# Kernel optimization log

Hardware: AMD Instinct MI355X
Metric: run time of the kernel (lower is better)

The kernel has to match this reference:

```python
import jax, jax.numpy as jnp
import numpy as np

M = 12          # persons per frame
K = 2           # partition channels from conv1da (1024 = 2*512)
D = 512         # GCN channel dim / LSTM hidden
C_IN = 4096     # backbone feature dim
NUM_CLASSES = 8


def setup_inputs() -> dict:
    key = jax.random.key(0)
    ks = jax.random.split(key, 8)
    N, T = 16, 32
    NT = N * T
    base_out = jax.random.normal(ks[0], (NT, M, C_IN), dtype=jnp.float32)
    dist = jax.random.uniform(ks[1], (N, T, 3, K, M, M), dtype=jnp.float32)
    # conv1da: Conv1d(4096 -> 1024, k=1, bias=False) == matmul with [1024, 4096]
    w_a = jax.random.normal(ks[2], (K * D, C_IN), dtype=jnp.float32) * 0.02
    # LSTM(512, 512, 1): torch gate order i, f, g, o
    s = 1.0 / np.sqrt(D)
    w_ih = jax.random.uniform(ks[3], (4 * D, D), minval=-s, maxval=s, dtype=jnp.float32)
    w_hh = jax.random.uniform(ks[4], (4 * D, D), minval=-s, maxval=s, dtype=jnp.float32)
    b_ih = jax.random.uniform(ks[5], (4 * D,), minval=-s, maxval=s, dtype=jnp.float32)
    b_hh = jax.random.uniform(ks[6], (4 * D,), minval=-s, maxval=s, dtype=jnp.float32)
    # gclassifier: Linear(512 -> num_classes)
    w_cls = jax.random.normal(ks[7], (NUM_CLASSES, D), dtype=jnp.float32) * 0.01
    b_cls = jnp.zeros((NUM_CLASSES,), dtype=jnp.float32)
    return {"base_out": base_out, "dist": dist, "w_a": w_a,
            "w_ih": w_ih, "w_hh": w_hh, "b_ih": b_ih, "b_hh": b_hh,
            "w_cls": w_cls, "b_cls": b_cls, "n_videos": N}


def reference(base_out, dist, w_a, w_ih, w_hh, b_ih, b_hh, w_cls, b_cls, n_videos):
    NT = base_out.shape[0]
    N = n_videos
    T = NT // N
    # conv1da (1x1 conv, no bias): [NT, M, 4096] -> [NT, K*D, M] -> [NT, K, D, M]
    node1 = jnp.einsum('nmc,oc->nom', base_out, w_a).reshape(NT, K, D, M)
    # fused three-way adjacency aggregation: node1a + node1b + node1c
    A = (dist[:, :, 2] + dist[:, :, 1] + dist[:, :, 0]).reshape(NT, K, M, M)
    node = jnp.einsum('nkcv,nkvw->ncw', node1, A)  # [NT, D, M]
    node = jax.nn.relu(node)
    # AdaptiveAvgPool1d(1) over the M persons
    pooled = node.mean(axis=2)                      # [NT, D]
    seq = pooled.reshape(N, T, D)
    # torch nn.LSTM default batch_first=False: iterates over axis 0 (N), batch=T
    def step(carry, x_t):
        h, c = carry
        g = x_t @ w_ih.T + b_ih + h @ w_hh.T + b_hh  # [T, 4D]
        i, f, gg, o = jnp.split(g, 4, axis=-1)
        c = jax.nn.sigmoid(f) * c + jax.nn.sigmoid(i) * jnp.tanh(gg)
        h = jax.nn.sigmoid(o) * jnp.tanh(c)
        return (h, c), h
    h0 = jnp.zeros((T, D), dtype=seq.dtype)
    c0 = jnp.zeros((T, D), dtype=seq.dtype)
    _, hs = jax.lax.scan(step, (h0, c0), seq)       # [N, T, D]
    last = hs[:, -1, :]                              # video_feat[:, -1, :]
    return last @ w_cls.T + b_cls                    # [N, num_classes]
```

## Files before the change

### kernel.cpp

```cpp
#include <hip/hip_runtime.h>
#include <math.h>

#define MM 12
#define KK 2
#define DD 512
#define CIN 4096
#define NCLS 8
#define NV 16
#define TT 32

typedef unsigned long long u64;
typedef __attribute__((ext_vector_type(8))) __bf16 bf16x8;
typedef __attribute__((ext_vector_type(4))) float f32x4;

#define PART_F   0
#define POOLED_F 786432
#define TAGA_F   794624
#define TAGD_F   798720
#define HGLOB_F  799232
#define PART_KS_STRIDE (192 * 1024)

#define MFMA_BF16(A, B, C) __builtin_amdgcn_mfma_f32_16x16x32_bf16((A), (B), (C), 0, 0, 0)
#define LOADR(p)      __hip_atomic_load((p), __ATOMIC_RELAXED, __HIP_MEMORY_SCOPE_AGENT)
#define LOADACQ(p)    __hip_atomic_load((p), __ATOMIC_ACQUIRE, __HIP_MEMORY_SCOPE_AGENT)
#define STORER(p, v)  __hip_atomic_store((p), (v), __ATOMIC_RELAXED, __HIP_MEMORY_SCOPE_AGENT)
#define STOREREL(p, v) __hip_atomic_store((p), (v), __ATOMIC_RELEASE, __HIP_MEMORY_SCOPE_AGENT)

__global__ __launch_bounds__(256, 1) void k_gemm_pool(
    const float* __restrict__ base_out, const float* __restrict__ dist,
    const float* __restrict__ w_a,
    float* __restrict__ part, float* __restrict__ pooled,
    unsigned* __restrict__ tagA)
{
  const int wg = blockIdx.x;
  const int tid = threadIdx.x;

  __shared__ __align__(16) unsigned short Ah[16 * 40], Al[16 * 40];
  __shared__ __align__(16) unsigned short Bh[192 * 40], Bl[192 * 40];
  __shared__ float Asum_s[KK * MM * MM];

  {
    const int ks = wg >> 6, ot = wg & 63;
    const int cc0 = ks * 1024;
    const int wave = tid >> 6, lane = tid & 63;
    const int jf0 = wave * 3;

    const int sq = tid & 7;
    const int sr = tid >> 3;
    unsigned boff[6];
#pragma unroll
    for (int rep = 0; rep < 6; ++rep) {
      const int j = sr + 32 * rep;
      const int n = j / 12, m = j - n * 12;
      boff[rep] = (unsigned)(((n * TT + 31) * MM + m) * CIN + cc0 + sq * 4);
    }
    const bool aact = tid < 128;
    unsigned aoff = aact ? (unsigned)((ot * 16 + (tid >> 3)) * CIN + cc0 + sq * 4) : 0u;

    f32x4 acc0 = {0.f, 0.f, 0.f, 0.f}, acc1 = acc0, acc2 = acc0;

    float4 pa, pb[6];
    if (aact) pa = *(const float4*)&w_a[aoff];
#pragma unroll
    for (int rep = 0; rep < 6; ++rep) pb[rep] = *(const float4*)&base_out[boff[rep]];

    for (int st = 0; st < 32; ++st) {
      __syncthreads();
      if (aact) {
        const int idx = (tid >> 3) * 40 + sq * 4;
        unsigned ux = __float_as_uint(pa.x), uy = __float_as_uint(pa.y);
        unsigned uz = __float_as_uint(pa.z), uw = __float_as_uint(pa.w);
        *(uint2*)&Ah[idx] = make_uint2((ux >> 16) | (uy & 0xFFFF0000u),
                                       (uz >> 16) | (uw & 0xFFFF0000u));
        unsigned lx = __float_as_uint(pa.x - __uint_as_float(ux & 0xFFFF0000u));
        unsigned ly = __float_as_uint(pa.y - __uint_as_float(uy & 0xFFFF0000u));
        unsigned lz = __float_as_uint(pa.z - __uint_as_float(uz & 0xFFFF0000u));
        unsigned lw = __float_as_uint(pa.w - __uint_as_float(uw & 0xFFFF0000u));
        *(uint2*)&Al[idx] = make_uint2((lx >> 16) | (ly & 0xFFFF0000u),
                                       (lz >> 16) | (lw & 0xFFFF0000u));
      }
#pragma unroll
      for (int rep = 0; rep < 6; ++rep) {
        const int idx = (sr + 32 * rep) * 40 + sq * 4;
        unsigned ux = __float_as_uint(pb[rep].x), uy = __float_as_uint(pb[rep].y);
        unsigned uz = __float_as_uint(pb[rep].z), uw = __float_as_uint(pb[rep].w);
        *(uint2*)&Bh[idx] = make_uint2((ux >> 16) | (uy & 0xFFFF0000u),
                                       (uz >> 16) | (uw & 0xFFFF0000u));
        unsigned lx = __float_as_uint(pb[rep].x - __uint_as_float(ux & 0xFFFF0000u));
        unsigned ly = __float_as_uint(pb[rep].y - __uint_as_float(uy & 0xFFFF0000u));
        unsigned lz = __float_as_uint(pb[rep].z - __uint_as_float(uz & 0xFFFF0000u));
        unsigned lw = __float_as_uint(pb[rep].w - __uint_as_float(uw & 0xFFFF0000u));
        *(uint2*)&Bl[idx] = make_uint2((lx >> 16) | (ly & 0xFFFF0000u),
                                       (lz >> 16) | (lw & 0xFFFF0000u));
      }
      __syncthreads();
      if (st < 31) {
        aoff += 32;
        if (aact) pa = *(const float4*)&w_a[aoff];
#pragma unroll
        for (int rep = 0; rep < 6; ++rep) {
          boff[rep] += 32;
          pb[rep] = *(const float4*)&base_out[boff[rep]];
        }
      }
      const int koff = (lane >> 4) * 8;
      const int fra = (lane & 15) * 40 + koff;
      bf16x8 oh = *(const bf16x8*)&Ah[fra];
      bf16x8 ol = *(const bf16x8*)&Al[fra];
      {
        const int r0 = ((jf0 + 0) * 16 + (lane & 15)) * 40 + koff;
        bf16x8 jh = *(const bf16x8*)&Bh[r0], jl = *(const bf16x8*)&Bl[r0];
        acc0 = MFMA_BF16(jh, oh, acc0);
        acc0 = MFMA_BF16(jh, ol, acc0);
        acc0 = MFMA_BF16(jl, oh, acc0);
      }
      {
        const int r1 = ((jf0 + 1) * 16 + (lane & 15)) * 40 + koff;
        bf16x8 jh = *(const bf16x8*)&Bh[r1], jl = *(const bf16x8*)&Bl[r1];
        acc1 = MFMA_BF16(jh, oh, acc1);
        acc1 = MFMA_BF16(jh, ol, acc1);
        acc1 = MFMA_BF16(jl, oh, acc1);
      }
      {
        const int r2 = ((jf0 + 2) * 16 + (lane & 15)) * 40 + koff;
        bf16x8 jh = *(const bf16x8*)&Bh[r2], jl = *(const bf16x8*)&Bl[r2];
        acc2 = MFMA_BF16(jh, oh, acc2);
        acc2 = MFMA_BF16(jh, ol, acc2);
        acc2 = MFMA_BF16(jl, oh, acc2);
      }
    }
    const int o = ot * 16 + (lane & 15);
    const int jr = (lane >> 4) * 4;
#pragma unroll
    for (int r = 0; r < 4; ++r) {
      part[((size_t)ks * 192 + (jf0 + 0) * 16 + jr + r) * 1024 + o] = acc0[r];
      part[((size_t)ks * 192 + (jf0 + 1) * 16 + jr + r) * 1024 + o] = acc1[r];
      part[((size_t)ks * 192 + (jf0 + 2) * 16 + jr + r) * 1024 + o] = acc2[r];
    }
    __syncthreads();
    if (tid == 0) STOREREL(&tagA[wg * 16], 1u);
  }

  if (tid < 64) {
    bool done;
    do {
      unsigned a0 = LOADR(&tagA[(tid      ) * 16]);
      unsigned a1 = LOADR(&tagA[(tid +  64) * 16]);
      unsigned a2 = LOADR(&tagA[(tid + 128) * 16]);
      unsigned a3 = LOADR(&tagA[(tid + 192) * 16]);
      done = __all(a0 == 1u && a1 == 1u && a2 == 1u && a3 == 1u);
    } while (!done);
  }
  __syncthreads();
  (void)LOADACQ(&tagA[0]);

  {
    const int n = wg >> 4, cb = (wg & 15) * 32;
    const unsigned dbase = (unsigned)((n * TT + 31) * (3 * KK * MM * MM));
    for (int f = tid; f < KK * MM * MM; f += 256)
      Asum_s[f] = dist[dbase + f] + dist[dbase + KK * MM * MM + f]
                + dist[dbase + 2 * KK * MM * MM + f];
    __syncthreads();
    if (tid < 32) {
      const int c = cb + tid;
      float nd[KK][MM];
#pragma unroll
      for (int k = 0; k < KK; ++k)
#pragma unroll
        for (int v = 0; v < MM; ++v) {
          const size_t off = (size_t)(n * MM + v) * 1024 + k * DD + c;
          nd[k][v] = part[off] + part[off + PART_KS_STRIDE]
                   + part[off + 2 * PART_KS_STRIDE] + part[off + 3 * PART_KS_STRIDE];
        }
      float accm = 0.f;
#pragma unroll
      for (int w = 0; w < MM; ++w) {
        float sw = 0.f;
#pragma unroll
        for (int k = 0; k < KK; ++k)
#pragma unroll
          for (int v = 0; v < MM; ++v) sw += nd[k][v] * Asum_s[(k * MM + v) * MM + w];
        accm += fmaxf(sw, 0.f);
      }
      pooled[n * DD + c] = accm * (1.f / 12.f);
    }
  }
}

__global__ __launch_bounds__(1024, 4) void k_lstm(
    const float* __restrict__ pooled,
    const float* __restrict__ w_ih, const float* __restrict__ w_hh,
    const float* __restrict__ b_ih, const float* __restrict__ b_hh,
    const float* __restrict__ w_cls, const float* __restrict__ b_cls,
    unsigned* __restrict__ tagD, u64* __restrict__ hg64,
    float* __restrict__ out)
{
  const int wg = blockIdx.x;
  const int tid = threadIdx.x;

  __shared__ __align__(16) float whh_s[64][516];
  __shared__ float gx_s[16][64];
  __shared__ __align__(16) float h_s[DD];
  __shared__ float dot_s[64];

  float* scratch = &whh_s[0][0];

  for (int f = tid; f < NV * DD; f += 1024)
    scratch[(f >> 9) * 516 + (f & 511)] = pooled[f];
  __syncthreads();

  {
    const int n = tid & 15, r = tid >> 4;
    const int grow = (r >> 4) * DD + wg * 16 + (r & 15);
    const float4* wr = (const float4*)&w_ih[(size_t)grow * DD];
    const float4* pv = (const float4*)&scratch[n * 516];
    float a = 0.f;
#pragma unroll 8
    for (int q = 0; q < DD / 4; ++q) {
      float4 x = wr[q], y = pv[q];
      a += x.x * y.x + x.y * y.y + x.z * y.z + x.w * y.w;
    }
    gx_s[n][r] = a + b_ih[grow] + b_hh[grow];
  }
  __syncthreads();

  for (int f = tid; f < 64 * 128; f += 1024) {
    const int rr = f >> 7, c4 = (f & 127) * 4;
    const int grow = (rr >> 4) * DD + wg * 16 + (rr & 15);
    *(float4*)&whh_s[rr][c4] = *(const float4*)&w_hh[(size_t)grow * DD + c4];
  }
  __syncthreads();

  {
    float c_reg = 0.f;
    const int r = tid >> 4;
    const int lj = tid & 15;

    for (int s = 0; s < NV; ++s) {
      if (s == 0) {
        if (tid < DD) h_s[tid] = 0.f;
      } else {
        if (tid < 64) {
          bool done;
          do {
            int t0 = (int)LOADR(&tagD[(tid & 31) * 16]);
            done = __all(t0 >= s);
          } while (!done);
        }
        __syncthreads();
        if (tid < DD) {
          u64 v = LOADR(&hg64[(size_t)(s - 1) * DD + tid]);
          while ((unsigned)v != (unsigned)s)
            v = LOADR(&hg64[(size_t)(s - 1) * DD + tid]);
          h_s[tid] = __uint_as_float((unsigned)(v >> 32));
        }
      }
      __syncthreads();

      float p = 0.f;
      const float4* wrow = (const float4*)&whh_s[r][0];
      const float4* hv4 = (const float4*)h_s;
#pragma unroll
      for (int q = 0; q < 8; ++q) {
        float4 wv = wrow[lj + 16 * q];
        float4 hv = hv4[lj + 16 * q];
        p += wv.x * hv.x + wv.y * hv.y + wv.z * hv.z + wv.w * hv.w;
      }
#pragma unroll
      for (int off = 8; off; off >>= 1) p += __shfl_down(p, off, 16);
      if (lj == 0) dot_s[r] = p;
      __syncthreads();

      if (tid < 16) {
        const float pi = gx_s[s][tid]      + dot_s[tid];
        const float pf = gx_s[s][16 + tid] + dot_s[16 + tid];
        const float pg = gx_s[s][32 + tid] + dot_s[32 + tid];
        const float po = gx_s[s][48 + tid] + dot_s[48 + tid];
        const float si = 1.f / (1.f + expf(-pi));
        const float sf = 1.f / (1.f + expf(-pf));
        const float so = 1.f / (1.f + expf(-po));
        c_reg = sf * c_reg + si * tanhf(pg);
        const float hn = so * tanhf(c_reg);
        const u64 pk = ((u64)__float_as_uint(hn) << 32) | (u64)(unsigned)(s + 1);
        STORER(&hg64[(size_t)s * DD + wg * 16 + tid], pk);
      }
      if (tid == 0) STORER(&tagD[wg * 16], (unsigned)(s + 1));
    }
  }

  if (wg == 0) {
    if (tid < 64) {
      bool done;
      do {
        int t0 = (int)LOADR(&tagD[(tid & 31) * 16]);
        done = __all(t0 >= NV);
      } while (!done);
    }
    __syncthreads();
    if (tid < DD) {
      u64 vv[NV];
#pragma unroll
      for (int n = 0; n < NV; ++n) vv[n] = LOADR(&hg64[(size_t)n * DD + tid]);
#pragma unroll
      for (int n = 0; n < NV; ++n) {
        u64 v = vv[n];
        while ((unsigned)v != (unsigned)(n + 1))
          v = LOADR(&hg64[(size_t)n * DD + tid]);
        scratch[n * 516 + tid] = __uint_as_float((unsigned)(v >> 32));
      }
    }
    __syncthreads();
    if (tid < NV * NCLS) {
      const int n = tid >> 3, cl = tid & 7;
      const float4* hv = (const float4*)&scratch[n * 516];
      const float4* wv = (const float4*)(w_cls + (size_t)cl * DD);
      float a = b_cls[cl];
#pragma unroll 8
      for (int q = 0; q < DD / 4; ++q) {
        float4 x = hv[q], y = wv[q];
        a += x.x * y.x + x.y * y.y + x.z * y.z + x.w * y.w;
      }
      out[tid] = a;
    }
  }
}

extern "C" void kernel_launch(void* const* d_in, const int* in_sizes, int n_in,
                              void* d_out, int out_size, void* d_ws, size_t ws_size,
                              hipStream_t stream) {
  const float* base_out = (const float*)d_in[0];
  const float* dist     = (const float*)d_in[1];
  const float* w_a      = (const float*)d_in[2];
  const float* w_ih     = (const float*)d_in[3];
  const float* w_hh     = (const float*)d_in[4];
  const float* b_ih     = (const float*)d_in[5];
  const float* b_hh     = (const float*)d_in[6];
  const float* w_cls    = (const float*)d_in[7];
  const float* b_cls    = (const float*)d_in[8];
  float* out = (float*)d_out;

  float* ws = (float*)d_ws;
  float* part   = ws + PART_F;
  float* pooled = ws + POOLED_F;
  unsigned* tagA = (unsigned*)(ws + TAGA_F);
  unsigned* tagD = (unsigned*)(ws + TAGD_F);
  u64* hg64 = (u64*)(ws + HGLOB_F);

  k_gemm_pool<<<dim3(256), 256, 0, stream>>>(base_out, dist, w_a, part, pooled, tagA);
  k_lstm<<<dim3(32), 1024, 0, stream>>>(pooled, w_ih, w_hh, b_ih, b_hh,
                                        w_cls, b_cls, tagD, hg64, out);
}
```

Measured before the change: 292.1 us.

## Drop per-block LSTM tag barrier; poll tagged h values directly and overlap weight loads

Removes the tagD counter array and the wave-level poll on all 32 block tags before each LSTM step. Each thread now spins only on its own tagged h element, with four loads unrolled per poll iteration. The w_hh shared-memory load is moved ahead of the w_ih input projection, which now reads pooled straight from global memory, cutting one __syncthreads and the pooled staging copy. The h stores become release stores, so the fine-grained polling stays correct without the separate tag write. The intent is to shorten the per-step inter-block synchronisation latency on the serial LSTM critical path, at the cost of more global polling traffic.

```diff
diff --git a/kernel.cpp b/kernel.cpp
--- a/kernel.cpp
+++ b/kernel.cpp
@@ -16,7 +16,6 @@
 #define PART_F   0
 #define POOLED_F 786432
 #define TAGA_F   794624
-#define TAGD_F   798720
 #define HGLOB_F  799232
 #define PART_KS_STRIDE (192 * 1024)
 
@@ -192,8 +191,7 @@
     const float* __restrict__ w_ih, const float* __restrict__ w_hh,
     const float* __restrict__ b_ih, const float* __restrict__ b_hh,
     const float* __restrict__ w_cls, const float* __restrict__ b_cls,
-    unsigned* __restrict__ tagD, u64* __restrict__ hg64,
-    float* __restrict__ out)
+    u64* __restrict__ hg64, float* __restrict__ out)
 {
   const int wg = blockIdx.x;
   const int tid = threadIdx.x;
@@ -203,17 +201,16 @@
   __shared__ __align__(16) float h_s[DD];
   __shared__ float dot_s[64];
 
-  float* scratch = &whh_s[0][0];
-
-  for (int f = tid; f < NV * DD; f += 1024)
-    scratch[(f >> 9) * 516 + (f & 511)] = pooled[f];
-  __syncthreads();
-
+  for (int f = tid; f < 64 * 128; f += 1024) {
+    const int rr = f >> 7, c4 = (f & 127) * 4;
+    const int grow = (rr >> 4) * DD + wg * 16 + (rr & 15);
+    *(float4*)&whh_s[rr][c4] = *(const float4*)&w_hh[(size_t)grow * DD + c4];
+  }
   {
-    const int n = tid & 15, r = tid >> 4;
+    const int n = tid >> 6, r = tid & 63;
     const int grow = (r >> 4) * DD + wg * 16 + (r & 15);
     const float4* wr = (const float4*)&w_ih[(size_t)grow * DD];
-    const float4* pv = (const float4*)&scratch[n * 516];
+    const float4* pv = (const float4*)&pooled[(size_t)n * DD];
     float a = 0.f;
 #pragma unroll 8
     for (int q = 0; q < DD / 4; ++q) {
@@ -224,13 +221,6 @@
   }
   __syncthreads();
 
-  for (int f = tid; f < 64 * 128; f += 1024) {
-    const int rr = f >> 7, c4 = (f & 127) * 4;
-    const int grow = (rr >> 4) * DD + wg * 16 + (rr & 15);
-    *(float4*)&whh_s[rr][c4] = *(const float4*)&w_hh[(size_t)grow * DD + c4];
-  }
-  __syncthreads();
-
   {
     float c_reg = 0.f;
     const int r = tid >> 4;
@@ -240,18 +230,19 @@
       if (s == 0) {
         if (tid < DD) h_s[tid] = 0.f;
       } else {
-        if (tid < 64) {
-          bool done;
-          do {
-            int t0 = (int)LOADR(&tagD[(tid & 31) * 16]);
-            done = __all(t0 >= s);
-          } while (!done);
-        }
-        __syncthreads();
         if (tid < DD) {
-          u64 v = LOADR(&hg64[(size_t)(s - 1) * DD + tid]);
-          while ((unsigned)v != (unsigned)s)
-            v = LOADR(&hg64[(size_t)(s - 1) * DD + tid]);
+          const u64* p = &hg64[(size_t)(s - 1) * DD + tid];
+          u64 v = LOADR(p);
+          while ((unsigned)v != (unsigned)s) {
+            u64 a0 = LOADR(p);
+            u64 a1 = LOADR(p);
+            u64 a2 = LOADR(p);
+            u64 a3 = LOADR(p);
+            if ((unsigned)a0 == (unsigned)s)      v = a0;
+            else if ((unsigned)a1 == (unsigned)s) v = a1;
+            else if ((unsigned)a2 == (unsigned)s) v = a2;
+            else                                  v = a3;
+          }
           h_s[tid] = __uint_as_float((unsigned)(v >> 32));
         }
       }
@@ -282,21 +273,13 @@
         c_reg = sf * c_reg + si * tanhf(pg);
         const float hn = so * tanhf(c_reg);
         const u64 pk = ((u64)__float_as_uint(hn) << 32) | (u64)(unsigned)(s + 1);
-        STORER(&hg64[(size_t)s * DD + wg * 16 + tid], pk);
-      }
-      if (tid == 0) STORER(&tagD[wg * 16], (unsigned)(s + 1));
+        STOREREL(&hg64[(size_t)s * DD + wg * 16 + tid], pk);
+      }
     }
   }
 
   if (wg == 0) {
-    if (tid < 64) {
-      bool done;
-      do {
-        int t0 = (int)LOADR(&tagD[(tid & 31) * 16]);
-        done = __all(t0 >= NV);
-      } while (!done);
-    }
-    __syncthreads();
+    float* scratch = &whh_s[0][0];
     if (tid < DD) {
       u64 vv[NV];
 #pragma unroll
@@ -343,10 +326,9 @@
   float* part   = ws + PART_F;
   float* pooled = ws + POOLED_F;
   unsigned* tagA = (unsigned*)(ws + TAGA_F);
-  unsigned* tagD = (unsigned*)(ws + TAGD_F);
   u64* hg64 = (u64*)(ws + HGLOB_F);
 
   k_gemm_pool<<<dim3(256), 256, 0, stream>>>(base_out, dist, w_a, part, pooled, tagA);
   k_lstm<<<dim3(32), 1024, 0, stream>>>(pooled, w_ih, w_hh, b_ih, b_hh,
-                                        w_cls, b_cls, tagD, hg64, out);
+                                        w_cls, b_cls, hg64, out);
 }
```

Result: slower. 339.1 us (+16.1%).
